# Kernel tuning notes

Measured on AMD Instinct MI355X. Metric: run time of the kernel, lower is better.

## Reference

```python
import jax, jax.numpy as jnp
import numpy as np

N, R, D, U, A = 200000, 4, 128, 32, 16  # entities, relations, embed, edge-embed, attention dims
E, K = 131072, 10                        # edges, neighbors per edge endpoint


def setup_inputs() -> dict:
    key = jax.random.key(0)
    ks = jax.random.split(key, 8)
    emd_std = 1.0 / np.sqrt(D)
    return {
        "edge_index": jax.random.randint(ks[0], (2, E), 0, N),
        "edge_attr": jax.random.uniform(ks[1], (E, R), dtype=jnp.float32),
        "n": jax.random.randint(ks[2], (2, E, K), 0, N),
        "emb": jax.random.uniform(ks[3], (N, D), minval=-1.0, maxval=1.0, dtype=jnp.float32),
        "u": jax.random.uniform(ks[4], (N, R, U), minval=-1.0, maxval=1.0, dtype=jnp.float32),
        "W": jnp.fmod(jax.random.normal(ks[5], (R, U, A), dtype=jnp.float32) * emd_std, 2.0),
        "w": jnp.fmod(jax.random.normal(ks[6], (R, A), dtype=jnp.float32) * emd_std, 2.0),
        "M": jnp.fmod(jax.random.normal(ks[7], (R, U, D), dtype=jnp.float32) * emd_std, 2.0),
    }


def _pipeline(entities, neighbors, edge_attr, emb, u, W, w, M):
    b = emb[entities]                                   # [E, D]
    u_r = jnp.mean(u[neighbors], axis=1)                # [E, K, R, U] -> [E, R, U]
    W_r = jnp.einsum('ir,rua->iua', edge_attr, W)       # [E, U, A]
    w_r = edge_attr @ w                                 # [E, A]
    scores = jnp.einsum('ira,ia->ir', jnp.tanh(jnp.einsum('iru,iua->ira', u_r, W_r)), w_r)
    attention = jax.nn.softmax(scores, axis=1)          # [E, R]
    # e = b + einsum('iue,iru,ir->ie', M_r, u_r, att) with M_r = einsum('ir,rue->iue').
    # Factored to avoid materializing M_r [E,U,D]: v[i,u] = sum_r u_r*att, then contract with M.
    v = jnp.einsum('iru,ir->iu', u_r, attention)        # [E, U]
    return b + jnp.einsum('ir,iu,rud->id', edge_attr, v, M)


def _l2_normalize(x, eps=1e-12):
    norm = jnp.sqrt(jnp.sum(x * x, axis=-1, keepdims=True))
    return x / jnp.maximum(norm, eps)


def reference(edge_index, edge_attr, n, emb, u, W, w, M):
    e_s = _pipeline(edge_index[0], n[0], edge_attr, emb, u, W, w, M)
    e_t = _pipeline(edge_index[1], n[1], edge_attr, emb, u, W, w, M)
    edge_emb = jnp.stack((e_s, e_t), axis=0)            # [2, E, D]
    return _l2_normalize(edge_emb)
```

## Files before the change

kernel.cpp:

```cpp
#include <hip/hip_runtime.h>

#define E_EDGES 131072
#define K_NB    10
#define D_DIM   128
#define U_DIM   32
#define A_DIM   16
#define R_DIM   4

#define EPG     4
#define WAVES   16
#define BLOCK   (WAVES * 64)
#define NGROUPS ((2 * E_EDGES) / EPG)
#define NBLOCKS (NGROUPS / WAVES)

__device__ __forceinline__ float frcp(float x) { return __builtin_amdgcn_rcpf(x); }

__device__ __forceinline__ float fast_tanh(float x) {
    x = fminf(fmaxf(x, -10.f), 10.f);
    const float t = __expf(2.f * x);
    return (t - 1.f) * frcp(t + 1.f);
}

__global__ __launch_bounds__(BLOCK, 4)
void gatne_fused(const int*   __restrict__ edge_index,
                 const float* __restrict__ edge_attr,
                 const int*   __restrict__ nbr,
                 const float* __restrict__ emb,
                 const float* __restrict__ u,
                 const float* __restrict__ Wt,
                 const float* __restrict__ wt,
                 const float* __restrict__ Mt,
                 float*       __restrict__ out)
{
    __shared__ float M_lds[R_DIM * U_DIM * D_DIM];
    __shared__ float ur_lds[WAVES][D_DIM];
    __shared__ float coef_lds[WAVES][EPG][D_DIM];

    const int tid = threadIdx.x;

    #pragma unroll
    for (int j = 0; j < (R_DIM * U_DIM * D_DIM) / (BLOCK * 4); ++j) {
        const int o = (j * BLOCK + tid) * 4;
        *reinterpret_cast<float4*>(&M_lds[o]) =
            *reinterpret_cast<const float4*>(&Mt[o]);
    }
    __syncthreads();

    const int wave = tid >> 6;
    const int lane = tid & 63;
    const int grp  = blockIdx.x * WAVES + wave;
    const int es0  = grp * EPG;
    const int side = es0 / E_EDGES;
    const int i0   = es0 - side * E_EDGES;

    const int rl = lane >> 4;
    const int al = lane & 15;

    float Wreg[U_DIM];
    #pragma unroll
    for (int uu = 0; uu < U_DIM; ++uu)
        Wreg[uu] = Wt[(rl * U_DIM + uu) * A_DIM + al];
    const float wreg0 = wt[0 * A_DIM + al];
    const float wreg1 = wt[1 * A_DIM + al];
    const float wreg2 = wt[2 * A_DIM + al];
    const float wreg3 = wt[3 * A_DIM + al];

    int idxA = 0;
    if (lane < EPG * K_NB) idxA = nbr[es0 * K_NB + lane];
    int entv = 0;
    if (lane < EPG)        entv = edge_index[es0 + lane];
    float attrv = 0.f;
    if (lane < EPG * R_DIM) attrv = edge_attr[i0 * R_DIM + lane];

    float* urp = ur_lds[wave];
    float* cfp = &coef_lds[wave][0][0];

    float2 b2[EPG];

    #pragma unroll
    for (int e = 0; e < EPG; ++e) {
        const float at0 = __shfl(attrv, e * 4 + 0);
        const float at1 = __shfl(attrv, e * 4 + 1);
        const float at2 = __shfl(attrv, e * 4 + 2);
        const float at3 = __shfl(attrv, e * 4 + 3);
        const int   ent = __shfl(entv, e);
        const float atm = (rl == 0) ? at0 : (rl == 1) ? at1 : (rl == 2) ? at2 : at3;

        float2 vals[K_NB];
        #pragma unroll
        for (int k = 0; k < K_NB; ++k) {
            const int node = __shfl(idxA, e * K_NB + k);
            vals[k] = *reinterpret_cast<const float2*>(&u[node * D_DIM + 2 * lane]);
        }
        b2[e] = *reinterpret_cast<const float2*>(&emb[ent * D_DIM + 2 * lane]);

        float sx = 0.f, sy = 0.f;
        #pragma unroll
        for (int k = 0; k < K_NB; ++k) { sx += vals[k].x; sy += vals[k].y; }
        sx *= 0.1f; sy *= 0.1f;
        *reinterpret_cast<float2*>(&urp[2 * lane]) = make_float2(sx, sy);

        const float wr = at0 * wreg0 + at1 * wreg1 + at2 * wreg2 + at3 * wreg3;

        float sc[R_DIM];
        #pragma unroll
        for (int r = 0; r < R_DIM; ++r) {
            float g = 0.f;
            #pragma unroll
            for (int u4 = 0; u4 < U_DIM / 4; ++u4) {
                const float4 uv =
                    *reinterpret_cast<const float4*>(&urp[r * U_DIM + u4 * 4]);
                g += uv.x * Wreg[u4 * 4 + 0];
                g += uv.y * Wreg[u4 * 4 + 1];
                g += uv.z * Wreg[u4 * 4 + 2];
                g += uv.w * Wreg[u4 * 4 + 3];
            }
            float v0 = atm * g;
            v0 += __shfl_xor(v0, 16);
            v0 += __shfl_xor(v0, 32);
            float t = fast_tanh(v0) * wr;
            t += __shfl_xor(t, 1);
            t += __shfl_xor(t, 2);
            t += __shfl_xor(t, 4);
            t += __shfl_xor(t, 8);
            sc[r] = t;
        }

        const float mx  = fmaxf(fmaxf(sc[0], sc[1]), fmaxf(sc[2], sc[3]));
        const float ex0 = __expf(sc[0] - mx), ex1 = __expf(sc[1] - mx);
        const float ex2 = __expf(sc[2] - mx), ex3 = __expf(sc[3] - mx);
        const float inv = frcp(ex0 + ex1 + ex2 + ex3);
        const float a0 = ex0 * inv, a1 = ex1 * inv, a2 = ex2 * inv, a3 = ex3 * inv;

        const int ub = (2 * lane) & 31;
        const float vA = a0 * urp[0 * U_DIM + ub]     + a1 * urp[1 * U_DIM + ub] +
                         a2 * urp[2 * U_DIM + ub]     + a3 * urp[3 * U_DIM + ub];
        const float vB = a0 * urp[0 * U_DIM + ub + 1] + a1 * urp[1 * U_DIM + ub + 1] +
                         a2 * urp[2 * U_DIM + ub + 1] + a3 * urp[3 * U_DIM + ub + 1];
        *reinterpret_cast<float2*>(&cfp[e * D_DIM + 2 * lane]) =
            make_float2(atm * vA, atm * vB);
    }

    float2 acc[EPG];
    #pragma unroll
    for (int e = 0; e < EPG; ++e) { acc[e].x = 0.f; acc[e].y = 0.f; }

    for (int c = 0; c < (R_DIM * U_DIM) / 4; ++c) {
        float4 cf4[EPG];
        #pragma unroll
        for (int e = 0; e < EPG; ++e)
            cf4[e] = *reinterpret_cast<const float4*>(&cfp[e * D_DIM + c * 4]);
        #pragma unroll
        for (int jj = 0; jj < 4; ++jj) {
            const float2 m2 = *reinterpret_cast<const float2*>(
                &M_lds[(c * 4 + jj) * D_DIM + 2 * lane]);
            #pragma unroll
            for (int e = 0; e < EPG; ++e) {
                const float cv = (jj == 0) ? cf4[e].x : (jj == 1) ? cf4[e].y
                               : (jj == 2) ? cf4[e].z : cf4[e].w;
                acc[e].x += cv * m2.x;
                acc[e].y += cv * m2.y;
            }
        }
    }

    #pragma unroll
    for (int e = 0; e < EPG; ++e) {
        const float ox = b2[e].x + acc[e].x;
        const float oy = b2[e].y + acc[e].y;
        float ss = ox * ox + oy * oy;
        ss += __shfl_xor(ss, 1);
        ss += __shfl_xor(ss, 2);
        ss += __shfl_xor(ss, 4);
        ss += __shfl_xor(ss, 8);
        ss += __shfl_xor(ss, 16);
        ss += __shfl_xor(ss, 32);
        const float scale = frcp(fmaxf(sqrtf(ss), 1e-12f));
        *reinterpret_cast<float2*>(&out[(es0 + e) * D_DIM + 2 * lane]) =
            make_float2(ox * scale, oy * scale);
    }
}

extern "C" void kernel_launch(void* const* d_in, const int* in_sizes, int n_in,
                              void* d_out, int out_size, void* d_ws, size_t ws_size,
                              hipStream_t stream)
{
    const int*   edge_index = (const int*)  d_in[0];
    const float* edge_attr  = (const float*)d_in[1];
    const int*   nbr        = (const int*)  d_in[2];
    const float* emb        = (const float*)d_in[3];
    const float* u          = (const float*)d_in[4];
    const float* Wt         = (const float*)d_in[5];
    const float* wt         = (const float*)d_in[6];
    const float* Mt         = (const float*)d_in[7];
    float*       out        = (float*)d_out;

    gatne_fused<<<dim3(NBLOCKS), dim3(BLOCK), 0, stream>>>(
        edge_index, edge_attr, nbr, emb, u, Wt, wt, Mt, out);
}
```

Before: 654.9 us.

## Hoist all neighbor gathers before compute and stage W through LDS

All 40 neighbor rows and 4 embedding rows for the wave's edges are now gathered up front, before any per-edge compute, so more global loads are in flight at once. The gathered values are summed as they arrive rather than buffered per edge. W is staged once per block into shared memory in a lane-friendly layout, and its register copy is loaded only after the gathers, which cuts register pressure during the load phase. The occupancy hint moves from a launch-bounds minimum to an explicit waves-per-EU attribute. The risk is that more outstanding loads and the accumulators raise VGPR use and change the achieved occupancy.

```diff
diff --git a/kernel.cpp b/kernel.cpp
--- a/kernel.cpp
+++ b/kernel.cpp
@@ -21,7 +21,7 @@
     return (t - 1.f) * frcp(t + 1.f);
 }
 
-__global__ __launch_bounds__(BLOCK, 4)
+__global__ __launch_bounds__(BLOCK) __attribute__((amdgpu_waves_per_eu(4, 4)))
 void gatne_fused(const int*   __restrict__ edge_index,
                  const float* __restrict__ edge_attr,
                  const int*   __restrict__ nbr,
@@ -33,6 +33,7 @@
                  float*       __restrict__ out)
 {
     __shared__ float M_lds[R_DIM * U_DIM * D_DIM];
+    __shared__ float W_lds[U_DIM * 64];
     __shared__ float ur_lds[WAVES][D_DIM];
     __shared__ float coef_lds[WAVES][EPG][D_DIM];
 
@@ -43,6 +44,13 @@
         const int o = (j * BLOCK + tid) * 4;
         *reinterpret_cast<float4*>(&M_lds[o]) =
             *reinterpret_cast<const float4*>(&Mt[o]);
+    }
+    #pragma unroll
+    for (int j = 0; j < (U_DIM * 64) / BLOCK; ++j) {
+        const int idx = j * BLOCK + tid;
+        const int uu  = idx >> 6;
+        const int ln  = idx & 63;
+        W_lds[idx] = Wt[((ln >> 4) * U_DIM + uu) * A_DIM + (ln & 15)];
     }
     __syncthreads();
 
@@ -56,10 +64,6 @@
     const int rl = lane >> 4;
     const int al = lane & 15;
 
-    float Wreg[U_DIM];
-    #pragma unroll
-    for (int uu = 0; uu < U_DIM; ++uu)
-        Wreg[uu] = Wt[(rl * U_DIM + uu) * A_DIM + al];
     const float wreg0 = wt[0 * A_DIM + al];
     const float wreg1 = wt[1 * A_DIM + al];
     const float wreg2 = wt[2 * A_DIM + al];
@@ -76,6 +80,28 @@
     float* cfp = &coef_lds[wave][0][0];
 
     float2 b2[EPG];
+    float2 s[EPG];
+    #pragma unroll
+    for (int e = 0; e < EPG; ++e) {
+        const int ent = __shfl(entv, e);
+        b2[e] = *reinterpret_cast<const float2*>(&emb[ent * D_DIM + 2 * lane]);
+        s[e] = make_float2(0.f, 0.f);
+    }
+    #pragma unroll
+    for (int e = 0; e < EPG; ++e) {
+        #pragma unroll
+        for (int k = 0; k < K_NB; ++k) {
+            const int node = __shfl(idxA, e * K_NB + k);
+            const float2 v =
+                *reinterpret_cast<const float2*>(&u[node * D_DIM + 2 * lane]);
+            s[e].x += v.x; s[e].y += v.y;
+        }
+    }
+
+    float Wreg[U_DIM];
+    #pragma unroll
+    for (int uu = 0; uu < U_DIM; ++uu)
+        Wreg[uu] = W_lds[uu * 64 + lane];
 
     #pragma unroll
     for (int e = 0; e < EPG; ++e) {
@@ -83,22 +109,10 @@
         const float at1 = __shfl(attrv, e * 4 + 1);
         const float at2 = __shfl(attrv, e * 4 + 2);
         const float at3 = __shfl(attrv, e * 4 + 3);
-        const int   ent = __shfl(entv, e);
         const float atm = (rl == 0) ? at0 : (rl == 1) ? at1 : (rl == 2) ? at2 : at3;
 
-        float2 vals[K_NB];
-        #pragma unroll
-        for (int k = 0; k < K_NB; ++k) {
-            const int node = __shfl(idxA, e * K_NB + k);
-            vals[k] = *reinterpret_cast<const float2*>(&u[node * D_DIM + 2 * lane]);
-        }
-        b2[e] = *reinterpret_cast<const float2*>(&emb[ent * D_DIM + 2 * lane]);
-
-        float sx = 0.f, sy = 0.f;
-        #pragma unroll
-        for (int k = 0; k < K_NB; ++k) { sx += vals[k].x; sy += vals[k].y; }
-        sx *= 0.1f; sy *= 0.1f;
-        *reinterpret_cast<float2*>(&urp[2 * lane]) = make_float2(sx, sy);
+        *reinterpret_cast<float2*>(&urp[2 * lane]) =
+            make_float2(s[e].x * 0.1f, s[e].y * 0.1f);
 
         const float wr = at0 * wreg0 + at1 * wreg1 + at2 * wreg2 + at3 * wreg3;
 
```

New measurement: 688.9 us. 5.2% more time.
